# Optimization experiments

Measured on AMD Instinct MI355X. Metric: run time of the kernel, lower is better.

## Reference

```python
import jax, jax.numpy as jnp
import numpy as np


def conv1x1(x, W, b):
    # 1x1 Conv2d == per-pixel linear over channels. x: [B,C,H,W], W: [O,C], b: [O]
    return jnp.einsum('oc,bchw->bohw', W, x) + b[None, :, None, None]


def setup_inputs() -> dict:
    key = jax.random.key(0)
    ks = jax.random.split(key, 18)
    B, C, Hd, H, W = 16, 64, 64, 32, 32
    s = 0.05
    f = jax.random.normal
    return {
        'h': f(ks[0], (B, C, H, W), jnp.float32),
        'm': f(ks[1], (B, C, H, W), jnp.float32),
        'Wq': f(ks[2], (Hd, C), jnp.float32) * s,
        'bq': f(ks[3], (Hd,), jnp.float32) * s,
        'Wk': f(ks[4], (Hd, C), jnp.float32) * s,
        'bk': f(ks[5], (Hd,), jnp.float32) * s,
        'Wk2': f(ks[6], (Hd, C), jnp.float32) * s,
        'bk2': f(ks[7], (Hd,), jnp.float32) * s,
        'Wv': f(ks[8], (C, C), jnp.float32) * s,
        'bv': f(ks[9], (C,), jnp.float32) * s,
        'Wv2': f(ks[10], (C, C), jnp.float32) * s,
        'bv2': f(ks[11], (C,), jnp.float32) * s,
        'Wz': f(ks[12], (2 * C, 2 * C), jnp.float32) * s,
        'bz': f(ks[13], (2 * C,), jnp.float32) * s,
        'Wm': f(ks[14], (3 * C, 3 * C), jnp.float32) * s,
        'bm': f(ks[15], (3 * C,), jnp.float32) * s,
    }


def reference(h, m, Wq, bq, Wk, bk, Wk2, bk2, Wv, bv, Wv2, bv2, Wz, bz, Wm, bm):
    B, C, H, W = h.shape
    Hd = Wq.shape[0]
    N = H * W
    # Shared query from h
    Q_h = conv1x1(h, Wq, bq).reshape(B, Hd, N).transpose(0, 2, 1)  # [B,N,Hd]
    # Self-attention branch over h
    K_h = conv1x1(h, Wk, bk).reshape(B, Hd, N)                     # [B,Hd,N]
    A_h = jax.nn.softmax(jnp.einsum('bnd,bdm->bnm', Q_h, K_h), axis=-1)  # [B,N,N]
    V_h = conv1x1(h, Wv, bv).reshape(B, C, N)                      # [B,C,N]
    Z_h = jnp.einsum('bnm,bcm->bcn', A_h, V_h).reshape(B, C, H, W)
    # Cross-attention branch over memory m (same query Q_h)
    K_m = conv1x1(m, Wk2, bk2).reshape(B, Hd, N)
    A_m = jax.nn.softmax(jnp.einsum('bnd,bdm->bnm', Q_h, K_m), axis=-1)
    V_m = conv1x1(m, Wv2, bv2).reshape(B, C, N)
    Z_m = jnp.einsum('bnm,bcm->bcn', A_m, V_m).reshape(B, C, H, W)
    # Fuse and gated memory update
    Z = conv1x1(jnp.concatenate([Z_h, Z_m], axis=1), Wz, bz)       # [B,2C,H,W]
    combined = conv1x1(jnp.concatenate([Z, h], axis=1), Wm, bm)    # [B,3C,H,W]
    mo, mg, mi = combined[:, :C], combined[:, C:2 * C], combined[:, 2 * C:]
    mi = jax.nn.sigmoid(mi)
    new_m = (1 - mi) * m + mi * jnp.tanh(mg)
    new_h = jax.nn.sigmoid(mo) * new_m
    return (new_h, new_m)
```

## Files before the change

kernel.cpp:

```cpp
#include <hip/hip_runtime.h>

typedef unsigned short u16;
typedef unsigned int u32;
typedef __attribute__((ext_vector_type(8))) short bf16x8;
typedef __attribute__((ext_vector_type(4))) short bf16x4;
typedef __attribute__((ext_vector_type(4))) float f32x4;

#define MFMA(a, b, c) __builtin_amdgcn_mfma_f32_16x16x32_bf16((a), (b), (c), 0, 0, 0)
#define MFMA16(a, b, c) __builtin_amdgcn_mfma_f32_16x16x16bf16_1k((a), (b), (c), 0, 0, 0)

static __device__ __forceinline__ u16 f2bf(float x) {
  u32 u = __float_as_uint(x);
  u += 0x7FFFu + ((u >> 16) & 1u);
  return (u16)(u >> 16);
}
static __device__ __forceinline__ u32 packbf_t(float hi, float lo) {
  return __builtin_amdgcn_perm(__float_as_uint(hi), __float_as_uint(lo), 0x07060302u);
}
static __device__ __forceinline__ u32 packbf(float lo, float hi) {
  return (u32)f2bf(lo) | ((u32)f2bf(hi) << 16);
}

__global__ void prep_kernel(const float* __restrict__ Wq, const float* __restrict__ Wk,
                            const float* __restrict__ Wk2, const float* __restrict__ Wv,
                            const float* __restrict__ Wv2, const float* __restrict__ Wz,
                            const float* __restrict__ Wm, const float* __restrict__ bm,
                            u16* __restrict__ W5, u16* __restrict__ Wzb,
                            u16* __restrict__ Wmb, float* __restrict__ bmp) {
  const int id = blockIdx.x * 256 + threadIdx.x;
  if (id < 20480) {
    const int wi = id >> 12, e = id & 4095;
    const float* src = wi == 0 ? Wq : wi == 1 ? Wk : wi == 2 ? Wk2 : wi == 3 ? Wv : Wv2;
    W5[id] = f2bf(src[e]);
  } else if (id < 36864) {
    const int e = id - 20480;
    Wzb[e] = f2bf(Wz[e]);
  } else if (id < 73728) {
    const int e = id - 36864;
    const int p = e / 192, k = e % 192;
    const int hb2 = p / 96, r1 = p % 96, ctl = r1 / 48, r2 = r1 % 48;
    const int g = r2 >> 4, mm = r2 & 15;
    const int o = g * 64 + (hb2 * 2 + ctl) * 16 + mm;
    Wmb[p * 192 + k] = f2bf(Wm[o * 192 + k]);
  } else if (id < 73920) {
    const int p = id - 73728;
    const int hb2 = p / 96, r1 = p % 96, ctl = r1 / 48, r2 = r1 % 48;
    const int g = r2 >> 4, mm = r2 & 15;
    const int o = g * 64 + (hb2 * 2 + ctl) * 16 + mm;
    bmp[p] = bm[o];
  }
}

__global__ __launch_bounds__(256) void proj_kernel(
    const float* __restrict__ h, const float* __restrict__ m_,
    const float* __restrict__ bq, const float* __restrict__ bk,
    const float* __restrict__ bk2, const float* __restrict__ bv,
    const float* __restrict__ bv2, const u16* __restrict__ W5,
    u16* __restrict__ Qb, u16* __restrict__ Khb, u16* __restrict__ Kmb,
    u16* __restrict__ Vhb, u16* __restrict__ Vmb, u16* __restrict__ hbuf)
{
  const int b = blockIdx.y, n0 = blockIdx.x * 64, z = blockIdx.z;
  __shared__ __align__(16) u16 xt[64][72];
  const int tid = threadIdx.x;
  const float* __restrict__ X = z ? m_ : h;

  {
    const int px = tid & 63, c0 = (tid >> 6) * 16;
#pragma unroll
    for (int i = 0; i < 8; ++i) {
      const int c = c0 + 2 * i;
      const float f0 = X[(b * 64 + c) * 1024 + n0 + px];
      const float f1 = X[(b * 64 + c + 1) * 1024 + n0 + px];
      *(u32*)&xt[px][c] = packbf(f0, f1);
    }
  }
  __syncthreads();

  const int lane = tid & 63, w = tid >> 6;
  const int mm = lane & 15, q = lane >> 4;

  const bf16x8 xa0 = *(const bf16x8*)&xt[w * 16 + mm][q * 8];
  const bf16x8 xa1 = *(const bf16x8*)&xt[w * 16 + mm][32 + q * 8];

  auto qk_store = [&](u16* dst, const u16* Wb, const float* bias) {
#pragma unroll
    for (int ot = 0; ot < 4; ++ot) {
      const bf16x8 wb0 = *(const bf16x8*)(Wb + (ot * 16 + mm) * 64 + q * 8);
      const bf16x8 wb1 = *(const bf16x8*)(Wb + (ot * 16 + mm) * 64 + 32 + q * 8);
      const float4 b4 = *(const float4*)(bias + ot * 16 + q * 4);
      f32x4 d = {b4.x, b4.y, b4.z, b4.w};
      d = MFMA(wb0, xa0, d);
      d = MFMA(wb1, xa1, d);
      uint2 val;
      val.x = packbf(d[0], d[1]);
      val.y = packbf(d[2], d[3]);
      *(uint2*)(dst + (b * 1024 + n0 + w * 16 + mm) * 64 + ot * 16 + q * 4) = val;
    }
  };
  auto v_store = [&](u16* dst, const u16* Wb, const float* bias) {
#pragma unroll
    for (int ot = 0; ot < 4; ++ot) {
      const bf16x8 wb0 = *(const bf16x8*)(Wb + (ot * 16 + mm) * 64 + q * 8);
      const bf16x8 wb1 = *(const bf16x8*)(Wb + (ot * 16 + mm) * 64 + 32 + q * 8);
      const float bb = bias[ot * 16 + mm];
      f32x4 d = {bb, bb, bb, bb};
      d = MFMA(xa0, wb0, d);
      d = MFMA(xa1, wb1, d);
      uint2 val;
      val.x = packbf(d[0], d[1]);
      val.y = packbf(d[2], d[3]);
      *(uint2*)(dst + b * 65536 + blockIdx.x * 4096 + (ot * 16 + mm) * 64 +
                w * 16 + q * 4) = val;
    }
  };

  if (z == 0) {
    qk_store(Qb, W5, bq);
    qk_store(Khb, W5 + 4096, bk);
    v_store(Vhb, W5 + 3 * 4096, bv);
    const int px = tid >> 2, sg = tid & 3;
    u32* dst = (u32*)(hbuf + (b * 1024 + n0 + px) * 64 + sg * 16);
    const u16* srcr = &xt[px][sg * 16];
#pragma unroll
    for (int j = 0; j < 8; ++j) dst[j] = *(const u32*)(srcr + 2 * j);
  } else {
    qk_store(Kmb, W5 + 2 * 4096, bk2);
    v_store(Vmb, W5 + 4 * 4096, bv2);
  }
}

__global__ __launch_bounds__(256) void attn_kernel(
    const u16* __restrict__ Qb, const u16* __restrict__ Khb,
    const u16* __restrict__ Kmb, const u16* __restrict__ Vhb,
    const u16* __restrict__ Vmb, u16* __restrict__ Ztb)
{
  const int id = blockIdx.x;
  const int b = id & 15;
  const int br = (id >> 4) & 1;
  const int qh = id >> 5;
  const u16* __restrict__ K = (br ? Kmb : Khb) + b * 65536;
  const u16* __restrict__ V = (br ? Vmb : Vhb) + b * 65536;

  __shared__ __align__(16) u16 pool[18432];
  __shared__ float rsw[4][64];
  u16* const Kl = pool;
  u16* const Vl = pool + 9216;

  const int tid = threadIdx.x, w = tid >> 6, lane = tid & 63;
  const int mm = lane & 15, q = lane >> 4;
  const int q0 = qh * 64;

  bf16x8 qb0[4], qb1[4];
#pragma unroll
  for (int qt = 0; qt < 4; ++qt) {
    const u16* Qp = Qb + (b * 1024 + q0 + qt * 16 + mm) * 64;
    qb0[qt] = *(const bf16x8*)(Qp + q * 8);
    qb1[qt] = *(const bf16x8*)(Qp + 32 + q * 8);
  }

  f32x4 z[4][4];
#pragma unroll
  for (int qt = 0; qt < 4; ++qt)
#pragma unroll
    for (int ct = 0; ct < 4; ++ct) z[qt][ct] = (f32x4){0.f, 0.f, 0.f, 0.f};
  float rp[4] = {0.f, 0.f, 0.f, 0.f};

  const int so0 = (tid >> 3) * 72 + (tid & 7) * 8;
  const int so1 = so0 + 32 * 72;
  uint4 sk0, sk1, sv0, sv1;
  auto stage_load = [&](int kc) {
    const u16* Ks = K + kc * 4096;
    const u16* Vs = V + kc * 4096;
    sk0 = *(const uint4*)(Ks + tid * 8);
    sk1 = *(const uint4*)(Ks + tid * 8 + 2048);
    sv0 = *(const uint4*)(Vs + tid * 8);
    sv1 = *(const uint4*)(Vs + tid * 8 + 2048);
  };
  auto stage_store = [&](int buf) {
    u16* Kd = Kl + buf * 4608;
    u16* Vd = Vl + buf * 4608;
    *(uint4*)(Kd + so0) = sk0;
    *(uint4*)(Kd + so1) = sk1;
    *(uint4*)(Vd + so0) = sv0;
    *(uint4*)(Vd + so1) = sv1;
  };

  stage_load(0);
  stage_store(0);
  __syncthreads();

  int cur = 0;
#pragma unroll 1
  for (int kc = 0; kc < 16; ++kc) {
    if (kc < 15) stage_load(kc + 1);

    const u16* Kc = Kl + cur * 4608;
    const u16* Vc = Vl + cur * 4608;
    const bf16x8 kf0 = *(const bf16x8*)(Kc + (w * 16 + mm) * 72 + q * 8);
    const bf16x8 kf1 = *(const bf16x8*)(Kc + (w * 16 + mm) * 72 + 32 + q * 8);
    bf16x4 vf[4];
#pragma unroll
    for (int ct = 0; ct < 4; ++ct)
      vf[ct] = *(const bf16x4*)(Vc + (ct * 16 + mm) * 72 + w * 16 + q * 4);

#pragma unroll
    for (int qt = 0; qt < 4; ++qt) {
      f32x4 s = {0.f, 0.f, 0.f, 0.f};
      s = MFMA(kf0, qb0[qt], s);
      s = MFMA(kf1, qb1[qt], s);
      const float e0 = __expf(s[0]), e1 = __expf(s[1]);
      const float e2 = __expf(s[2]), e3 = __expf(s[3]);
      rp[qt] += (e0 + e1) + (e2 + e3);
      union { u32 u[2]; bf16x4 v; } pb;
      pb.u[0] = packbf_t(e1, e0);
      pb.u[1] = packbf_t(e3, e2);
#pragma unroll
      for (int ct = 0; ct < 4; ++ct) z[qt][ct] = MFMA16(vf[ct], pb.v, z[qt][ct]);
    }

    if (kc < 15) stage_store(cur ^ 1);
    __syncthreads();
    cur ^= 1;
  }

  u16* const zcb = pool;
#pragma unroll
  for (int qt = 0; qt < 4; ++qt) {
    float v = rp[qt];
    v += __shfl_xor(v, 16);
    v += __shfl_xor(v, 32);
    if (q == 0) rsw[w][qt * 16 + mm] = v;
#pragma unroll
    for (int ct = 0; ct < 4; ++ct) {
      uint2 val;
      val.x = packbf_t(z[qt][ct][1], z[qt][ct][0]);
      val.y = packbf_t(z[qt][ct][3], z[qt][ct][2]);
      *(uint2*)(zcb + w * 4352 + (qt * 16 + mm) * 68 + ct * 16 + q * 4) = val;
    }
  }
  __syncthreads();

  const int c2 = tid & 31, qr = tid >> 5;
#pragma unroll
  for (int i = 0; i < 8; ++i) {
    const int query = qr + i * 8;
    const float rt = rsw[0][query] + rsw[1][query] + rsw[2][query] + rsw[3][query];
    const float rinv = __builtin_amdgcn_rcpf(rt);
    float vlo = 0.f, vhi = 0.f;
#pragma unroll
    for (int ww = 0; ww < 4; ++ww) {
      const u32 u = *(const u32*)(zcb + ww * 4352 + query * 68 + c2 * 2);
      vlo += __uint_as_float(u << 16);
      vhi += __uint_as_float(u & 0xffff0000u);
    }
    vlo *= rinv;
    vhi *= rinv;
    *(u32*)(Ztb + (b * 1024 + q0 + query) * 128 + br * 64 + c2 * 2) = packbf_t(vhi, vlo);
  }
}

__global__ __launch_bounds__(256) void tail_kernel(
    const u16* __restrict__ Ztb, const u16* __restrict__ hbuf,
    const float* __restrict__ m_, const u16* __restrict__ Wzb,
    const float* __restrict__ bz, const u16* __restrict__ Wmb,
    const float* __restrict__ bmp, float* __restrict__ out)
{
  const int b = blockIdx.y, n0 = blockIdx.x * 32;
  __shared__ __align__(16) u16 zp[32][136];
  const int tid = threadIdx.x, lane = tid & 63, wv = tid >> 6;
  const int mm = lane & 15, q = lane >> 4;
  const int pxt = wv & 1, oh = wv >> 1;

  {
    bf16x8 za[4];
#pragma unroll
    for (int ks = 0; ks < 4; ++ks)
      za[ks] = *(const bf16x8*)(Ztb + (b * 1024 + n0 + pxt * 16 + mm) * 128 +
                                ks * 32 + q * 8);
#pragma unroll
    for (int ot = 0; ot < 4; ++ot) {
      const int o0 = oh * 64 + ot * 16;
      const float4 b4 = *(const float4*)(bz + o0 + q * 4);
      f32x4 d = {b4.x, b4.y, b4.z, b4.w};
#pragma unroll
      for (int ks = 0; ks < 4; ++ks) {
        const bf16x8 wb = *(const bf16x8*)(Wzb + (o0 + mm) * 128 + ks * 32 + q * 8);
        d = MFMA(wb, za[ks], d);
      }
      uint2 val;
      val.x = packbf(d[0], d[1]);
      val.y = packbf(d[2], d[3]);
      *(uint2*)&zp[pxt * 16 + mm][o0 + q * 4] = val;
    }
  }
  __syncthreads();

  {
    const int hb2 = oh;
    bf16x8 fa[6];
#pragma unroll
    for (int ks = 0; ks < 4; ++ks)
      fa[ks] = *(const bf16x8*)&zp[pxt * 16 + mm][ks * 32 + q * 8];
    {
      const u16* hp = hbuf + (b * 1024 + n0 + pxt * 16 + mm) * 64;
      fa[4] = *(const bf16x8*)(hp + q * 8);
      fa[5] = *(const bf16x8*)(hp + 32 + q * 8);
    }
    f32x4 dd[6];
#pragma unroll
    for (int j = 0; j < 6; ++j) {
      const int p = hb2 * 96 + j * 16 + mm;
      const float bb = bmp[p];
      f32x4 d = {bb, bb, bb, bb};
#pragma unroll
      for (int ks = 0; ks < 6; ++ks) {
        const bf16x8 wb = *(const bf16x8*)(Wmb + p * 192 + ks * 32 + q * 8);
        d = MFMA(fa[ks], wb, d);
      }
      dd[j] = d;
    }
#pragma unroll
    for (int ctl = 0; ctl < 2; ++ctl) {
      const int c = (hb2 * 2 + ctl) * 16 + mm;
      const int px = n0 + pxt * 16 + q * 4;
      const float4 mold = *(const float4*)(m_ + (b * 64 + c) * 1024 + px);
      float4 nh, nm;
#pragma unroll
      for (int r = 0; r < 4; ++r) {
        const float xo = dd[ctl * 3 + 0][r];
        const float xg = dd[ctl * 3 + 1][r];
        const float xi = dd[ctl * 3 + 2][r];
        const float si = __builtin_amdgcn_rcpf(1.f + __expf(-xi));
        const float th = 1.f - 2.f * __builtin_amdgcn_rcpf(__expf(2.f * xg) + 1.f);
        const float so = __builtin_amdgcn_rcpf(1.f + __expf(-xo));
        const float mo = ((const float*)&mold)[r];
        const float nmv = (1.f - si) * mo + si * th;
        ((float*)&nm)[r] = nmv;
        ((float*)&nh)[r] = so * nmv;
      }
      *(float4*)(out + (b * 64 + c) * 1024 + px) = nh;
      *(float4*)(out + 1048576 + (b * 64 + c) * 1024 + px) = nm;
    }
  }
}

extern "C" void kernel_launch(void* const* d_in, const int* in_sizes, int n_in,
                              void* d_out, int out_size, void* d_ws, size_t ws_size,
                              hipStream_t stream) {
  const float* h   = (const float*)d_in[0];
  const float* m   = (const float*)d_in[1];
  const float* Wq  = (const float*)d_in[2];
  const float* bq  = (const float*)d_in[3];
  const float* Wk  = (const float*)d_in[4];
  const float* bk  = (const float*)d_in[5];
  const float* Wk2 = (const float*)d_in[6];
  const float* bk2 = (const float*)d_in[7];
  const float* Wv  = (const float*)d_in[8];
  const float* bv  = (const float*)d_in[9];
  const float* Wv2 = (const float*)d_in[10];
  const float* bv2 = (const float*)d_in[11];
  const float* Wz  = (const float*)d_in[12];
  const float* bz  = (const float*)d_in[13];
  const float* Wm  = (const float*)d_in[14];
  const float* bm  = (const float*)d_in[15];
  float* out = (float*)d_out;

  char* ws = (char*)d_ws;
  const size_t MB = 1024 * 1024;
  u16* Qb   = (u16*)(ws + 0 * MB);
  u16* Khb  = (u16*)(ws + 2 * MB);
  u16* Kmb  = (u16*)(ws + 4 * MB);
  u16* Vhb  = (u16*)(ws + 6 * MB);
  u16* Vmb  = (u16*)(ws + 8 * MB);
  u16* hbuf = (u16*)(ws + 10 * MB);
  u16* Ztb  = (u16*)(ws + 12 * MB);
  u16* W5   = (u16*)(ws + 16 * MB);
  u16* Wzb  = (u16*)(ws + 16 * MB + 40960);
  u16* Wmb  = (u16*)(ws + 16 * MB + 73728);
  float* bmp = (float*)(ws + 16 * MB + 147456);

  prep_kernel<<<289, 256, 0, stream>>>(Wq, Wk, Wk2, Wv, Wv2, Wz, Wm, bm,
                                       W5, Wzb, Wmb, bmp);
  proj_kernel<<<dim3(16, 16, 2), 256, 0, stream>>>(h, m, bq, bk, bk2, bv, bv2, W5,
                                                   Qb, Khb, Kmb, Vhb, Vmb, hbuf);
  attn_kernel<<<512, 256, 0, stream>>>(Qb, Khb, Kmb, Vhb, Vmb, Ztb);
  tail_kernel<<<dim3(32, 16), 256, 0, stream>>>(Ztb, hbuf, m, Wzb, bz, Wmb, bmp, out);
}
```

Baseline: 138.6 us.

## Fuse four kernels into one persistent kernel with grid barriers

Merges the weight-prep, projection, attention and tail kernels into a single 512-block launch, with atomic-counter grid barriers between phases. The goal is to drop three kernel launch gaps and their inter-kernel drain and ramp costs. It adds a memset per call, spin-wait barrier overhead, and relies on all 512 blocks being co-resident (launch bounds ask for 2 blocks per CU). If they are not all resident, the kernel would deadlock.

After: 288.7 us. +108.3%, slower.

```diff
diff --git a/kernel.cpp b/kernel.cpp
--- a/kernel.cpp
+++ b/kernel.cpp
@@ -21,325 +21,345 @@
   return (u32)f2bf(lo) | ((u32)f2bf(hi) << 16);
 }
 
-__global__ void prep_kernel(const float* __restrict__ Wq, const float* __restrict__ Wk,
-                            const float* __restrict__ Wk2, const float* __restrict__ Wv,
-                            const float* __restrict__ Wv2, const float* __restrict__ Wz,
-                            const float* __restrict__ Wm, const float* __restrict__ bm,
-                            u16* __restrict__ W5, u16* __restrict__ Wzb,
-                            u16* __restrict__ Wmb, float* __restrict__ bmp) {
-  const int id = blockIdx.x * 256 + threadIdx.x;
-  if (id < 20480) {
-    const int wi = id >> 12, e = id & 4095;
-    const float* src = wi == 0 ? Wq : wi == 1 ? Wk : wi == 2 ? Wk2 : wi == 3 ? Wv : Wv2;
-    W5[id] = f2bf(src[e]);
-  } else if (id < 36864) {
-    const int e = id - 20480;
-    Wzb[e] = f2bf(Wz[e]);
-  } else if (id < 73728) {
-    const int e = id - 36864;
-    const int p = e / 192, k = e % 192;
-    const int hb2 = p / 96, r1 = p % 96, ctl = r1 / 48, r2 = r1 % 48;
-    const int g = r2 >> 4, mm = r2 & 15;
-    const int o = g * 64 + (hb2 * 2 + ctl) * 16 + mm;
-    Wmb[p * 192 + k] = f2bf(Wm[o * 192 + k]);
-  } else if (id < 73920) {
-    const int p = id - 73728;
-    const int hb2 = p / 96, r1 = p % 96, ctl = r1 / 48, r2 = r1 % 48;
-    const int g = r2 >> 4, mm = r2 & 15;
-    const int o = g * 64 + (hb2 * 2 + ctl) * 16 + mm;
-    bmp[p] = bm[o];
-  }
-}
-
-__global__ __launch_bounds__(256) void proj_kernel(
-    const float* __restrict__ h, const float* __restrict__ m_,
-    const float* __restrict__ bq, const float* __restrict__ bk,
-    const float* __restrict__ bk2, const float* __restrict__ bv,
-    const float* __restrict__ bv2, const u16* __restrict__ W5,
-    u16* __restrict__ Qb, u16* __restrict__ Khb, u16* __restrict__ Kmb,
-    u16* __restrict__ Vhb, u16* __restrict__ Vmb, u16* __restrict__ hbuf)
-{
-  const int b = blockIdx.y, n0 = blockIdx.x * 64, z = blockIdx.z;
-  __shared__ __align__(16) u16 xt[64][72];
-  const int tid = threadIdx.x;
-  const float* __restrict__ X = z ? m_ : h;
-
-  {
-    const int px = tid & 63, c0 = (tid >> 6) * 16;
-#pragma unroll
-    for (int i = 0; i < 8; ++i) {
-      const int c = c0 + 2 * i;
-      const float f0 = X[(b * 64 + c) * 1024 + n0 + px];
-      const float f1 = X[(b * 64 + c + 1) * 1024 + n0 + px];
-      *(u32*)&xt[px][c] = packbf(f0, f1);
-    }
+static __device__ __forceinline__ void grid_barrier(u32* ctr, u32 nblk) {
+  __syncthreads();
+  if (threadIdx.x == 0) {
+    __threadfence();
+    __hip_atomic_fetch_add(ctr, 1u, __ATOMIC_RELEASE, __HIP_MEMORY_SCOPE_AGENT);
+    while (__hip_atomic_load(ctr, __ATOMIC_RELAXED, __HIP_MEMORY_SCOPE_AGENT) < nblk) {
+      __builtin_amdgcn_s_sleep(1);
+    }
+    __threadfence();
   }
   __syncthreads();
-
-  const int lane = tid & 63, w = tid >> 6;
-  const int mm = lane & 15, q = lane >> 4;
-
-  const bf16x8 xa0 = *(const bf16x8*)&xt[w * 16 + mm][q * 8];
-  const bf16x8 xa1 = *(const bf16x8*)&xt[w * 16 + mm][32 + q * 8];
-
-  auto qk_store = [&](u16* dst, const u16* Wb, const float* bias) {
-#pragma unroll
-    for (int ot = 0; ot < 4; ++ot) {
-      const bf16x8 wb0 = *(const bf16x8*)(Wb + (ot * 16 + mm) * 64 + q * 8);
-      const bf16x8 wb1 = *(const bf16x8*)(Wb + (ot * 16 + mm) * 64 + 32 + q * 8);
-      const float4 b4 = *(const float4*)(bias + ot * 16 + q * 4);
-      f32x4 d = {b4.x, b4.y, b4.z, b4.w};
-      d = MFMA(wb0, xa0, d);
-      d = MFMA(wb1, xa1, d);
-      uint2 val;
-      val.x = packbf(d[0], d[1]);
-      val.y = packbf(d[2], d[3]);
-      *(uint2*)(dst + (b * 1024 + n0 + w * 16 + mm) * 64 + ot * 16 + q * 4) = val;
-    }
-  };
-  auto v_store = [&](u16* dst, const u16* Wb, const float* bias) {
-#pragma unroll
-    for (int ot = 0; ot < 4; ++ot) {
-      const bf16x8 wb0 = *(const bf16x8*)(Wb + (ot * 16 + mm) * 64 + q * 8);
-      const bf16x8 wb1 = *(const bf16x8*)(Wb + (ot * 16 + mm) * 64 + 32 + q * 8);
-      const float bb = bias[ot * 16 + mm];
-      f32x4 d = {bb, bb, bb, bb};
-      d = MFMA(xa0, wb0, d);
-      d = MFMA(xa1, wb1, d);
-      uint2 val;
-      val.x = packbf(d[0], d[1]);
-      val.y = packbf(d[2], d[3]);
-      *(uint2*)(dst + b * 65536 + blockIdx.x * 4096 + (ot * 16 + mm) * 64 +
-                w * 16 + q * 4) = val;
-    }
-  };
-
-  if (z == 0) {
-    qk_store(Qb, W5, bq);
-    qk_store(Khb, W5 + 4096, bk);
-    v_store(Vhb, W5 + 3 * 4096, bv);
-    const int px = tid >> 2, sg = tid & 3;
-    u32* dst = (u32*)(hbuf + (b * 1024 + n0 + px) * 64 + sg * 16);
-    const u16* srcr = &xt[px][sg * 16];
-#pragma unroll
-    for (int j = 0; j < 8; ++j) dst[j] = *(const u32*)(srcr + 2 * j);
-  } else {
-    qk_store(Kmb, W5 + 2 * 4096, bk2);
-    v_store(Vmb, W5 + 4 * 4096, bv2);
+}
+
+__global__ __launch_bounds__(256, 2) void fused_kernel(
+    const float* __restrict__ h, const float* __restrict__ m_,
+    const float* __restrict__ Wq, const float* __restrict__ bq,
+    const float* __restrict__ Wk, const float* __restrict__ bk,
+    const float* __restrict__ Wk2, const float* __restrict__ bk2,
+    const float* __restrict__ Wv, const float* __restrict__ bv,
+    const float* __restrict__ Wv2, const float* __restrict__ bv2,
+    const float* __restrict__ Wz, const float* __restrict__ bz,
+    const float* __restrict__ Wm, const float* __restrict__ bm,
+    float* __restrict__ out,
+    u16* __restrict__ Qb, u16* __restrict__ Khb, u16* __restrict__ Kmb,
+    u16* __restrict__ Vhb, u16* __restrict__ Vmb, u16* __restrict__ hbuf,
+    u16* __restrict__ Ztb, u16* __restrict__ W5, u16* __restrict__ Wzb,
+    u16* __restrict__ Wmb, float* __restrict__ bmp, u32* __restrict__ bars)
+{
+  const int tid = threadIdx.x;
+  const int bid = blockIdx.x;
+
+  __shared__ __align__(16) u16 smem[18944];
+
+  {
+    const int id = bid * 256 + tid;
+    if (id < 20480) {
+      const int wi = id >> 12, e = id & 4095;
+      const float* src = wi == 0 ? Wq : wi == 1 ? Wk : wi == 2 ? Wk2 : wi == 3 ? Wv : Wv2;
+      W5[id] = f2bf(src[e]);
+    } else if (id < 36864) {
+      const int e = id - 20480;
+      Wzb[e] = f2bf(Wz[e]);
+    } else if (id < 73728) {
+      const int e = id - 36864;
+      const int p = e / 192, k = e % 192;
+      const int hb2 = p / 96, r1 = p % 96, ctl = r1 / 48, r2 = r1 % 48;
+      const int g = r2 >> 4, mm = r2 & 15;
+      const int o = g * 64 + (hb2 * 2 + ctl) * 16 + mm;
+      Wmb[p * 192 + k] = f2bf(Wm[o * 192 + k]);
+    } else if (id < 73920) {
+      const int p = id - 73728;
+      const int hb2 = p / 96, r1 = p % 96, ctl = r1 / 48, r2 = r1 % 48;
+      const int g = r2 >> 4, mm = r2 & 15;
+      const int o = g * 64 + (hb2 * 2 + ctl) * 16 + mm;
+      bmp[p] = bm[o];
+    }
   }
-}
-
-__global__ __launch_bounds__(256) void attn_kernel(
-    const u16* __restrict__ Qb, const u16* __restrict__ Khb,
-    const u16* __restrict__ Kmb, const u16* __restrict__ Vhb,
-    const u16* __restrict__ Vmb, u16* __restrict__ Ztb)
-{
-  const int id = blockIdx.x;
-  const int b = id & 15;
-  const int br = (id >> 4) & 1;
-  const int qh = id >> 5;
-  const u16* __restrict__ K = (br ? Kmb : Khb) + b * 65536;
-  const u16* __restrict__ V = (br ? Vmb : Vhb) + b * 65536;
-
-  __shared__ __align__(16) u16 pool[18432];
-  __shared__ float rsw[4][64];
-  u16* const Kl = pool;
-  u16* const Vl = pool + 9216;
-
-  const int tid = threadIdx.x, w = tid >> 6, lane = tid & 63;
-  const int mm = lane & 15, q = lane >> 4;
-  const int q0 = qh * 64;
-
-  bf16x8 qb0[4], qb1[4];
-#pragma unroll
-  for (int qt = 0; qt < 4; ++qt) {
-    const u16* Qp = Qb + (b * 1024 + q0 + qt * 16 + mm) * 64;
-    qb0[qt] = *(const bf16x8*)(Qp + q * 8);
-    qb1[qt] = *(const bf16x8*)(Qp + 32 + q * 8);
+
+  grid_barrier(bars + 0, 512);
+
+  {
+    const int n0 = (bid & 15) * 64;
+    const int b = (bid >> 4) & 15;
+    const int z = bid >> 8;
+    u16 (*xt)[72] = (u16(*)[72])smem;
+    const float* __restrict__ X = z ? m_ : h;
+
+    {
+      const int px = tid & 63, c0 = (tid >> 6) * 16;
+#pragma unroll
+      for (int i = 0; i < 8; ++i) {
+        const int c = c0 + 2 * i;
+        const float f0 = X[(b * 64 + c) * 1024 + n0 + px];
+        const float f1 = X[(b * 64 + c + 1) * 1024 + n0 + px];
+        *(u32*)&xt[px][c] = packbf(f0, f1);
+      }
+    }
+    __syncthreads();
+
+    const int lane = tid & 63, w = tid >> 6;
+    const int mm = lane & 15, q = lane >> 4;
+
+    const bf16x8 xa0 = *(const bf16x8*)&xt[w * 16 + mm][q * 8];
+    const bf16x8 xa1 = *(const bf16x8*)&xt[w * 16 + mm][32 + q * 8];
+
+    auto qk_store = [&](u16* dst, const u16* Wb, const float* bias) {
+#pragma unroll
+      for (int ot = 0; ot < 4; ++ot) {
+        const bf16x8 wb0 = *(const bf16x8*)(Wb + (ot * 16 + mm) * 64 + q * 8);
+        const bf16x8 wb1 = *(const bf16x8*)(Wb + (ot * 16 + mm) * 64 + 32 + q * 8);
+        const float4 b4 = *(const float4*)(bias + ot * 16 + q * 4);
+        f32x4 d = {b4.x, b4.y, b4.z, b4.w};
+        d = MFMA(wb0, xa0, d);
+        d = MFMA(wb1, xa1, d);
+        uint2 val;
+        val.x = packbf(d[0], d[1]);
+        val.y = packbf(d[2], d[3]);
+        *(uint2*)(dst + (b * 1024 + n0 + w * 16 + mm) * 64 + ot * 16 + q * 4) = val;
+      }
+    };
+    auto v_store = [&](u16* dst, const u16* Wb, const float* bias) {
+#pragma unroll
+      for (int ot = 0; ot < 4; ++ot) {
+        const bf16x8 wb0 = *(const bf16x8*)(Wb + (ot * 16 + mm) * 64 + q * 8);
+        const bf16x8 wb1 = *(const bf16x8*)(Wb + (ot * 16 + mm) * 64 + 32 + q * 8);
+        const float bb = bias[ot * 16 + mm];
+        f32x4 d = {bb, bb, bb, bb};
+        d = MFMA(xa0, wb0, d);
+        d = MFMA(xa1, wb1, d);
+        uint2 val;
+        val.x = packbf(d[0], d[1]);
+        val.y = packbf(d[2], d[3]);
+        *(uint2*)(dst + b * 65536 + (bid & 15) * 4096 + (ot * 16 + mm) * 64 +
+                  w * 16 + q * 4) = val;
+      }
+    };
+
+    if (z == 0) {
+      qk_store(Qb, W5, bq);
+      qk_store(Khb, W5 + 4096, bk);
+      v_store(Vhb, W5 + 3 * 4096, bv);
+      const int px = tid >> 2, sg = tid & 3;
+      u32* dst = (u32*)(hbuf + (b * 1024 + n0 + px) * 64 + sg * 16);
+      const u16* srcr = &xt[px][sg * 16];
+#pragma unroll
+      for (int j = 0; j < 8; ++j) dst[j] = *(const u32*)(srcr + 2 * j);
+    } else {
+      qk_store(Kmb, W5 + 2 * 4096, bk2);
+      v_store(Vmb, W5 + 4 * 4096, bv2);
+    }
   }
 
-  f32x4 z[4][4];
-#pragma unroll
-  for (int qt = 0; qt < 4; ++qt)
-#pragma unroll
-    for (int ct = 0; ct < 4; ++ct) z[qt][ct] = (f32x4){0.f, 0.f, 0.f, 0.f};
-  float rp[4] = {0.f, 0.f, 0.f, 0.f};
-
-  const int so0 = (tid >> 3) * 72 + (tid & 7) * 8;
-  const int so1 = so0 + 32 * 72;
-  uint4 sk0, sk1, sv0, sv1;
-  auto stage_load = [&](int kc) {
-    const u16* Ks = K + kc * 4096;
-    const u16* Vs = V + kc * 4096;
-    sk0 = *(const uint4*)(Ks + tid * 8);
-    sk1 = *(const uint4*)(Ks + tid * 8 + 2048);
-    sv0 = *(const uint4*)(Vs + tid * 8);
-    sv1 = *(const uint4*)(Vs + tid * 8 + 2048);
-  };
-  auto stage_store = [&](int buf) {
-    u16* Kd = Kl + buf * 4608;
-    u16* Vd = Vl + buf * 4608;
-    *(uint4*)(Kd + so0) = sk0;
-    *(uint4*)(Kd + so1) = sk1;
-    *(uint4*)(Vd + so0) = sv0;
-    *(uint4*)(Vd + so1) = sv1;
-  };
-
-  stage_load(0);
-  stage_store(0);
-  __syncthreads();
-
-  int cur = 0;
+  grid_barrier(bars + 1, 512);
+
+  {
+    const int id = bid;
+    const int b = id & 15;
+    const int br = (id >> 4) & 1;
+    const int qh = id >> 5;
+    const u16* __restrict__ K = (br ? Kmb : Khb) + b * 65536;
+    const u16* __restrict__ V = (br ? Vmb : Vhb) + b * 65536;
+
+    u16* const pool = smem;
+    float (*rsw)[64] = (float(*)[64])(smem + 18432);
+    u16* const Kl = pool;
+    u16* const Vl = pool + 9216;
+
+    const int w = tid >> 6, lane = tid & 63;
+    const int mm = lane & 15, q = lane >> 4;
+    const int q0 = qh * 64;
+
+    bf16x8 qb0[4], qb1[4];
+#pragma unroll
+    for (int qt = 0; qt < 4; ++qt) {
+      const u16* Qp = Qb + (b * 1024 + q0 + qt * 16 + mm) * 64;
+      qb0[qt] = *(const bf16x8*)(Qp + q * 8);
+      qb1[qt] = *(const bf16x8*)(Qp + 32 + q * 8);
+    }
+
+    f32x4 z[4][4];
+#pragma unroll
+    for (int qt = 0; qt < 4; ++qt)
+#pragma unroll
+      for (int ct = 0; ct < 4; ++ct) z[qt][ct] = (f32x4){0.f, 0.f, 0.f, 0.f};
+    float rp[4] = {0.f, 0.f, 0.f, 0.f};
+
+    const int so0 = (tid >> 3) * 72 + (tid & 7) * 8;
+    const int so1 = so0 + 32 * 72;
+    uint4 sk0, sk1, sv0, sv1;
+    auto stage_load = [&](int kc) {
+      const u16* Ks = K + kc * 4096;
+      const u16* Vs = V + kc * 4096;
+      sk0 = *(const uint4*)(Ks + tid * 8);
+      sk1 = *(const uint4*)(Ks + tid * 8 + 2048);
+      sv0 = *(const uint4*)(Vs + tid * 8);
+      sv1 = *(const uint4*)(Vs + tid * 8 + 2048);
+    };
+    auto stage_store = [&](int buf) {
+      u16* Kd = Kl + buf * 4608;
+      u16* Vd = Vl + buf * 4608;
+      *(uint4*)(Kd + so0) = sk0;
+      *(uint4*)(Kd + so1) = sk1;
+      *(uint4*)(Vd + so0) = sv0;
+      *(uint4*)(Vd + so1) = sv1;
+    };
+
+    stage_load(0);
+    stage_store(0);
+    __syncthreads();
+
+    int cur = 0;
 #pragma unroll 1
-  for (int kc = 0; kc < 16; ++kc) {
-    if (kc < 15) stage_load(kc + 1);
-
-    const u16* Kc = Kl + cur * 4608;
-    const u16* Vc = Vl + cur * 4608;
-    const bf16x8 kf0 = *(const bf16x8*)(Kc + (w * 16 + mm) * 72 + q * 8);
-    const bf16x8 kf1 = *(const bf16x8*)(Kc + (w * 16 + mm) * 72 + 32 + q * 8);
-    bf16x4 vf[4];
-#pragma unroll
-    for (int ct = 0; ct < 4; ++ct)
-      vf[ct] = *(const bf16x4*)(Vc + (ct * 16 + mm) * 72 + w * 16 + q * 4);
-
+    for (int kc = 0; kc < 16; ++kc) {
+      if (kc < 15) stage_load(kc + 1);
+
+      const u16* Kc = Kl + cur * 4608;
+      const u16* Vc = Vl + cur * 4608;
+      const bf16x8 kf0 = *(const bf16x8*)(Kc + (w * 16 + mm) * 72 + q * 8);
+      const bf16x8 kf1 = *(const bf16x8*)(Kc + (w * 16 + mm) * 72 + 32 + q * 8);
+      bf16x4 vf[4];
+#pragma unroll
+      for (int ct = 0; ct < 4; ++ct)
+        vf[ct] = *(const bf16x4*)(Vc + (ct * 16 + mm) * 72 + w * 16 + q * 4);
+
+#pragma unroll
+      for (int qt = 0; qt < 4; ++qt) {
+        f32x4 s = {0.f, 0.f, 0.f, 0.f};
+        s = MFMA(kf0, qb0[qt], s);
+        s = MFMA(kf1, qb1[qt], s);
+        const float e0 = __expf(s[0]), e1 = __expf(s[1]);
+        const float e2 = __expf(s[2]), e3 = __expf(s[3]);
+        rp[qt] += (e0 + e1) + (e2 + e3);
+        union { u32 u[2]; bf16x4 v; } pb;
+        pb.u[0] = packbf_t(e1, e0);
+        pb.u[1] = packbf_t(e3, e2);
+#pragma unroll
+        for (int ct = 0; ct < 4; ++ct) z[qt][ct] = MFMA16(vf[ct], pb.v, z[qt][ct]);
+      }
+
+      if (kc < 15) stage_store(cur ^ 1);
+      __syncthreads();
+      cur ^= 1;
+    }
+
+    u16* const zcb = pool;
 #pragma unroll
     for (int qt = 0; qt < 4; ++qt) {
-      f32x4 s = {0.f, 0.f, 0.f, 0.f};
-      s = MFMA(kf0, qb0[qt], s);
-      s = MFMA(kf1, qb1[qt], s);
-      const float e0 = __expf(s[0]), e1 = __expf(s[1]);
-      const float e2 = __expf(s[2]), e3 = __expf(s[3]);
-      rp[qt] += (e0 + e1) + (e2 + e3);
-      union { u32 u[2]; bf16x4 v; } pb;
-      pb.u[0] = packbf_t(e1, e0);
-      pb.u[1] = packbf_t(e3, e2);
-#pragma unroll
-      for (int ct = 0; ct < 4; ++ct) z[qt][ct] = MFMA16(vf[ct], pb.v, z[qt][ct]);
-    }
-
-    if (kc < 15) stage_store(cur ^ 1);
+      float v = rp[qt];
+      v += __shfl_xor(v, 16);
+      v += __shfl_xor(v, 32);
+      if (q == 0) rsw[w][qt * 16 + mm] = v;
+#pragma unroll
+      for (int ct = 0; ct < 4; ++ct) {
+        uint2 val;
+        val.x = packbf_t(z[qt][ct][1], z[qt][ct][0]);
+        val.y = packbf_t(z[qt][ct][3], z[qt][ct][2]);
+        *(uint2*)(zcb + w * 4352 + (qt * 16 + mm) * 68 + ct * 16 + q * 4) = val;
+      }
+    }
     __syncthreads();
-    cur ^= 1;
+
+    const int c2 = tid & 31, qr = tid >> 5;
+#pragma unroll
+    for (int i = 0; i < 8; ++i) {
+      const int query = qr + i * 8;
+      const float rt = rsw[0][query] + rsw[1][query] + rsw[2][query] + rsw[3][query];
+      const float rinv = __builtin_amdgcn_rcpf(rt);
+      float vlo = 0.f, vhi = 0.f;
+#pragma unroll
+      for (int ww = 0; ww < 4; ++ww) {
+        const u32 u = *(const u32*)(zcb + ww * 4352 + query * 68 + c2 * 2);
+        vlo += __uint_as_float(u << 16);
+        vhi += __uint_as_float(u & 0xffff0000u);
+      }
+      vlo *= rinv;
+      vhi *= rinv;
+      *(u32*)(Ztb + (b * 1024 + q0 + query) * 128 + br * 64 + c2 * 2) = packbf_t(vhi, vlo);
+    }
   }
 
-  u16* const zcb = pool;
-#pragma unroll
-  for (int qt = 0; qt < 4; ++qt) {
-    float v = rp[qt];
-    v += __shfl_xor(v, 16);
-    v += __shfl_xor(v, 32);
-    if (q == 0) rsw[w][qt * 16 + mm] = v;
-#pragma unroll
-    for (int ct = 0; ct < 4; ++ct) {
-      uint2 val;
-      val.x = packbf_t(z[qt][ct][1], z[qt][ct][0]);
-      val.y = packbf_t(z[qt][ct][3], z[qt][ct][2]);
-      *(uint2*)(zcb + w * 4352 + (qt * 16 + mm) * 68 + ct * 16 + q * 4) = val;
-    }
-  }
-  __syncthreads();
-
-  const int c2 = tid & 31, qr = tid >> 5;
-#pragma unroll
-  for (int i = 0; i < 8; ++i) {
-    const int query = qr + i * 8;
-    const float rt = rsw[0][query] + rsw[1][query] + rsw[2][query] + rsw[3][query];
-    const float rinv = __builtin_amdgcn_rcpf(rt);
-    float vlo = 0.f, vhi = 0.f;
-#pragma unroll
-    for (int ww = 0; ww < 4; ++ww) {
-      const u32 u = *(const u32*)(zcb + ww * 4352 + query * 68 + c2 * 2);
-      vlo += __uint_as_float(u << 16);
-      vhi += __uint_as_float(u & 0xffff0000u);
-    }
-    vlo *= rinv;
-    vhi *= rinv;
-    *(u32*)(Ztb + (b * 1024 + q0 + query) * 128 + br * 64 + c2 * 2) = packbf_t(vhi, vlo);
-  }
-}
-
-__global__ __launch_bounds__(256) void tail_kernel(
-    const u16* __restrict__ Ztb, const u16* __restrict__ hbuf,
-    const float* __restrict__ m_, const u16* __restrict__ Wzb,
-    const float* __restrict__ bz, const u16* __restrict__ Wmb,
-    const float* __restrict__ bmp, float* __restrict__ out)
-{
-  const int b = blockIdx.y, n0 = blockIdx.x * 32;
-  __shared__ __align__(16) u16 zp[32][136];
-  const int tid = threadIdx.x, lane = tid & 63, wv = tid >> 6;
-  const int mm = lane & 15, q = lane >> 4;
-  const int pxt = wv & 1, oh = wv >> 1;
+  grid_barrier(bars + 2, 512);
 
   {
-    bf16x8 za[4];
-#pragma unroll
-    for (int ks = 0; ks < 4; ++ks)
-      za[ks] = *(const bf16x8*)(Ztb + (b * 1024 + n0 + pxt * 16 + mm) * 128 +
-                                ks * 32 + q * 8);
-#pragma unroll
-    for (int ot = 0; ot < 4; ++ot) {
-      const int o0 = oh * 64 + ot * 16;
-      const float4 b4 = *(const float4*)(bz + o0 + q * 4);
-      f32x4 d = {b4.x, b4.y, b4.z, b4.w};
-#pragma unroll
-      for (int ks = 0; ks < 4; ++ks) {
-        const bf16x8 wb = *(const bf16x8*)(Wzb + (o0 + mm) * 128 + ks * 32 + q * 8);
-        d = MFMA(wb, za[ks], d);
-      }
-      uint2 val;
-      val.x = packbf(d[0], d[1]);
-      val.y = packbf(d[2], d[3]);
-      *(uint2*)&zp[pxt * 16 + mm][o0 + q * 4] = val;
-    }
-  }
-  __syncthreads();
-
-  {
-    const int hb2 = oh;
-    bf16x8 fa[6];
-#pragma unroll
-    for (int ks = 0; ks < 4; ++ks)
-      fa[ks] = *(const bf16x8*)&zp[pxt * 16 + mm][ks * 32 + q * 8];
+    const int b = bid >> 5, n0 = (bid & 31) * 32;
+    u16 (*zp)[136] = (u16(*)[136])smem;
+    const int lane = tid & 63, wv = tid >> 6;
+    const int mm = lane & 15, q = lane >> 4;
+    const int pxt = wv & 1, oh = wv >> 1;
+
     {
-      const u16* hp = hbuf + (b * 1024 + n0 + pxt * 16 + mm) * 64;
-      fa[4] = *(const bf16x8*)(hp + q * 8);
-      fa[5] = *(const bf16x8*)(hp + 32 + q * 8);
-    }
-    f32x4 dd[6];
-#pragma unroll
-    for (int j = 0; j < 6; ++j) {
-      const int p = hb2 * 96 + j * 16 + mm;
-      const float bb = bmp[p];
-      f32x4 d = {bb, bb, bb, bb};
-#pragma unroll
-      for (int ks = 0; ks < 6; ++ks) {
-        const bf16x8 wb = *(const bf16x8*)(Wmb + p * 192 + ks * 32 + q * 8);
-        d = MFMA(fa[ks], wb, d);
-      }
-      dd[j] = d;
-    }
-#pragma unroll
-    for (int ctl = 0; ctl < 2; ++ctl) {
-      const int c = (hb2 * 2 + ctl) * 16 + mm;
-      const int px = n0 + pxt * 16 + q * 4;
-      const float4 mold = *(const float4*)(m_ + (b * 64 + c) * 1024 + px);
-      float4 nh, nm;
-#pragma unroll
-      for (int r = 0; r < 4; ++r) {
-        const float xo = dd[ctl * 3 + 0][r];
-        const float xg = dd[ctl * 3 + 1][r];
-        const float xi = dd[ctl * 3 + 2][r];
-        const float si = __builtin_amdgcn_rcpf(1.f + __expf(-xi));
-        const float th = 1.f - 2.f * __builtin_amdgcn_rcpf(__expf(2.f * xg) + 1.f);
-        const float so = __builtin_amdgcn_rcpf(1.f + __expf(-xo));
-        const float mo = ((const float*)&mold)[r];
-        const float nmv = (1.f - si) * mo + si * th;
-        ((float*)&nm)[r] = nmv;
-        ((float*)&nh)[r] = so * nmv;
-      }
-      *(float4*)(out + (b * 64 + c) * 1024 + px) = nh;
-      *(float4*)(out + 1048576 + (b * 64 + c) * 1024 + px) = nm;
+      bf16x8 za[4];
+#pragma unroll
+      for (int ks = 0; ks < 4; ++ks)
+        za[ks] = *(const bf16x8*)(Ztb + (b * 1024 + n0 + pxt * 16 + mm) * 128 +
+                                  ks * 32 + q * 8);
+#pragma unroll
+      for (int ot = 0; ot < 4; ++ot) {
+        const int o0 = oh * 64 + ot * 16;
+        const float4 b4 = *(const float4*)(bz + o0 + q * 4);
+        f32x4 d = {b4.x, b4.y, b4.z, b4.w};
+#pragma unroll
+        for (int ks = 0; ks < 4; ++ks) {
+          const bf16x8 wb = *(const bf16x8*)(Wzb + (o0 + mm) * 128 + ks * 32 + q * 8);
+          d = MFMA(wb, za[ks], d);
+        }
+        uint2 val;
+        val.x = packbf(d[0], d[1]);
+        val.y = packbf(d[2], d[3]);
+        *(uint2*)&zp[pxt * 16 + mm][o0 + q * 4] = val;
+      }
+    }
+    __syncthreads();
+
+    {
+      const int hb2 = oh;
+      bf16x8 fa[6];
+#pragma unroll
+      for (int ks = 0; ks < 4; ++ks)
+        fa[ks] = *(const bf16x8*)&zp[pxt * 16 + mm][ks * 32 + q * 8];
+      {
+        const u16* hp = hbuf + (b * 1024 + n0 + pxt * 16 + mm) * 64;
+        fa[4] = *(const bf16x8*)(hp + q * 8);
+        fa[5] = *(const bf16x8*)(hp + 32 + q * 8);
+      }
+      f32x4 dd[6];
+#pragma unroll
+      for (int j = 0; j < 6; ++j) {
+        const int p = hb2 * 96 + j * 16 + mm;
+        const float bb = bmp[p];
+        f32x4 d = {bb, bb, bb, bb};
+#pragma unroll
+        for (int ks = 0; ks < 6; ++ks) {
+          const bf16x8 wb = *(const bf16x8*)(Wmb + p * 192 + ks * 32 + q * 8);
+          d = MFMA(fa[ks], wb, d);
+        }
+        dd[j] = d;
+      }
+#pragma unroll
+      for (int ctl = 0; ctl < 2; ++ctl) {
+        const int c = (hb2 * 2 + ctl) * 16 + mm;
+        const int px = n0 + pxt * 16 + q * 4;
+        const float4 mold = *(const float4*)(m_ + (b * 64 + c) * 1024 + px);
+        float4 nh, nm;
+#pragma unroll
+        for (int r = 0; r < 4; ++r) {
+          const float xo = dd[ctl * 3 + 0][r];
+          const float xg = dd[ctl * 3 + 1][r];
+          const float xi = dd[ctl * 3 + 2][r];
+          const float si = __builtin_amdgcn_rcpf(1.f + __expf(-xi));
+          const float th = 1.f - 2.f * __builtin_amdgcn_rcpf(__expf(2.f * xg) + 1.f);
+          const float so = __builtin_amdgcn_rcpf(1.f + __expf(-xo));
+          const float mo = ((const float*)&mold)[r];
+          const float nmv = (1.f - si) * mo + si * th;
+          ((float*)&nm)[r] = nmv;
+          ((float*)&nh)[r] = so * nmv;
+        }
+        *(float4*)(out + (b * 64 + c) * 1024 + px) = nh;
+        *(float4*)(out + 1048576 + (b * 64 + c) * 1024 + px) = nm;
+      }
     }
   }
 }
@@ -378,11 +398,11 @@
   u16* Wzb  = (u16*)(ws + 16 * MB + 40960);
   u16* Wmb  = (u16*)(ws + 16 * MB + 73728);
   float* bmp = (float*)(ws + 16 * MB + 147456);
-
-  prep_kernel<<<289, 256, 0, stream>>>(Wq, Wk, Wk2, Wv, Wv2, Wz, Wm, bm,
-                                       W5, Wzb, Wmb, bmp);
-  proj_kernel<<<dim3(16, 16, 2), 256, 0, stream>>>(h, m, bq, bk, bk2, bv, bv2, W5,
-                                                   Qb, Khb, Kmb, Vhb, Vmb, hbuf);
-  attn_kernel<<<512, 256, 0, stream>>>(Qb, Khb, Kmb, Vhb, Vmb, Ztb);
-  tail_kernel<<<dim3(32, 16), 256, 0, stream>>>(Ztb, hbuf, m, Wzb, bz, Wmb, bmp, out);
-}
+  u32* bars  = (u32*)(ws + 16 * MB + 148224);
+
+  hipMemsetAsync(bars, 0, 64, stream);
+  fused_kernel<<<512, 256, 0, stream>>>(h, m, Wq, bq, Wk, bk, Wk2, bk2, Wv, bv,
+                                        Wv2, bv2, Wz, bz, Wm, bm, out, Qb, Khb,
+                                        Kmb, Vhb, Vmb, hbuf, Ztb, W5, Wzb, Wmb,
+                                        bmp, bars);
+}
```
